# Optimization experiments

Measured on AMD Instinct MI355X. Metric: run time of the kernel, lower is better.

## Reference

```python
import jax, jax.numpy as jnp
import numpy as np

B, L, D, H = 2, 2048, 1024, 16
DK = D // H


def setup_inputs() -> dict:
    key = jax.random.key(0)
    ks = jax.random.split(key, 13)
    s = 1.0 / np.sqrt(D)
    return {
        "q": jax.random.normal(ks[0], (B, L, D), jnp.float32),
        "k": jax.random.normal(ks[1], (B, L, D), jnp.float32),
        "v": jax.random.normal(ks[2], (B, L, D), jnp.float32),
        "mask": jax.random.randint(ks[3], (B, L, L), 0, 2, jnp.int32),
        "Wq": jax.random.normal(ks[4], (D, D), jnp.float32) * s,
        "bq": jnp.zeros((D,), jnp.float32),
        "Wk": jax.random.normal(ks[5], (D, D), jnp.float32) * s,
        "bk": jnp.zeros((D,), jnp.float32),
        "Wv": jax.random.normal(ks[6], (D, D), jnp.float32) * s,
        "bv": jnp.zeros((D,), jnp.float32),
        "Wo": jax.random.normal(ks[7], (D, D), jnp.float32) * s,
        "bo": jnp.zeros((D,), jnp.float32),
    }


def reference(q, k, v, mask, Wq, bq, Wk, bk, Wv, bv, Wo, bo):
    # projections: [B, L, D] -> [B, L, H, DK]
    qh = (q @ Wq + bq).reshape(B, L, H, DK)
    kh = (k @ Wk + bk).reshape(B, L, H, DK)
    vh = (v @ Wv + bv).reshape(B, L, H, DK)
    # scores scaled by d_model (module passes model_dim=d_model, not sqrt(d_k))
    attn = jnp.einsum("bqhd,bkhd->bhqk", qh, kh) / D
    attn = jnp.where(mask[:, None, :, :] == 0, jnp.float32(-1e9), attn)
    attn = jax.nn.softmax(attn, axis=-1)  # [B, H, Lq, Lk]
    ctx = jnp.einsum("bhqk,bkhd->bqhd", attn, vh)  # [B, Lq, H, DK]
    out = ctx.reshape(B, L, D) @ Wo + bo
    # original returns attn flattened head-major: [H*B, Lq, Lk]
    attn_out = attn.transpose(1, 0, 2, 3).reshape(H * B, L, L)
    return out, attn_out
```

## Files before the change

kernel.cpp:

```cpp
#include <hip/hip_runtime.h>
#include <cstdint>

typedef unsigned short u16;
typedef unsigned long long u64;
typedef __attribute__((ext_vector_type(8))) short short8;
typedef __attribute__((ext_vector_type(4))) float floatx4;

#define DEV __device__ __forceinline__

#define GLD16(gp, lp)                                                          \
  __builtin_amdgcn_global_load_lds(                                            \
      (const __attribute__((address_space(1))) void*)(gp),                     \
      (__attribute__((address_space(3))) void*)(lp), 16, 0, 0)

DEV u16 f2bf(float f) {
  union { float f; uint32_t u; } x; x.f = f;
  uint32_t r = x.u + 0x7fffu + ((x.u >> 16) & 1u);
  return (u16)(r >> 16);
}


__global__ __launch_bounds__(256) void pack_mask(
    const int* __restrict__ mask, u64* __restrict__ mw) {
  const int lane = threadIdx.x & 63;
  int gw = (blockIdx.x * 256 + threadIdx.x) >> 6;
  const int nwaves = (gridDim.x * 256) >> 6;
  const int total = (2 * 2048 * 2048) / 64;
  for (int c = gw; c < total; c += nwaves) {
    int v = mask[(size_t)c * 64 + lane];
    u64 b = __ballot(v != 0);
    if (lane == 0) mw[c] = b;
  }
}

__global__ __launch_bounds__(256) void transpose_w(
    const float* __restrict__ s0, const float* __restrict__ s1,
    const float* __restrict__ s2, const float* __restrict__ s3,
    u16* __restrict__ d0, u16* __restrict__ d1,
    u16* __restrict__ d2, u16* __restrict__ d3) {
  const float* S; u16* D;
  switch (blockIdx.z) {
    case 0: S = s0; D = d0; break;
    case 1: S = s1; D = d1; break;
    case 2: S = s2; D = d2; break;
    default: S = s3; D = d3; break;
  }
  __shared__ u16 t[64][68];
  const int tid = threadIdx.x;
  const int r0 = blockIdx.y * 64, c0 = blockIdx.x * 64;
#pragma unroll
  for (int i = 0; i < 4; ++i) {
    int idx = i * 256 + tid;
    int r = idx >> 4, c = (idx & 15) * 4;
    float4 v = *(const float4*)(S + (size_t)(r0 + r) * 1024 + c0 + c);
    t[r][c] = f2bf(v.x); t[r][c + 1] = f2bf(v.y);
    t[r][c + 2] = f2bf(v.z); t[r][c + 3] = f2bf(v.w);
  }
  __syncthreads();
#pragma unroll
  for (int i = 0; i < 4; ++i) {
    int idx = i * 256 + tid;
    int r = idx >> 4, c = (idx & 15) * 4;
    ushort4 v;
    v.x = t[c][r]; v.y = t[c + 1][r]; v.z = t[c + 2][r]; v.w = t[c + 3][r];
    *(ushort4*)(D + (size_t)(c0 + r) * 1024 + r0 + c) = v;
  }
}

__global__ __launch_bounds__(256) void cvt3(
    const float* __restrict__ q, const float* __restrict__ k,
    const float* __restrict__ v, u16* __restrict__ dst) {
  const float* S = (blockIdx.z == 0) ? q : (blockIdx.z == 1) ? k : v;
  u16* D = dst + (size_t)blockIdx.z * (4u << 20);
  int i = (blockIdx.x * 256 + threadIdx.x) * 4;
  float4 val = *(const float4*)(S + i);
  ushort4 o;
  o.x = f2bf(val.x); o.y = f2bf(val.y); o.z = f2bf(val.z); o.w = f2bf(val.w);
  *(ushort4*)(D + i) = o;
}

__global__ __launch_bounds__(256, 3) void gemm_k(
    const u16* xb3, const u16* wts,
    const float* __restrict__ bq, const float* __restrict__ bk,
    const float* __restrict__ bv, const float* __restrict__ bo,
    u16* __restrict__ qh, u16* __restrict__ kh, u16* __restrict__ vt,
    const u16* ctx, float* __restrict__ out, int phase) {
  __shared__ __align__(16) u16 As[128 * 64];
  __shared__ __align__(16) u16 Bs[128 * 64];
  const int tid = threadIdx.x;
  const int wave = tid >> 6, lane = tid & 63;
  const int quad = lane >> 4, l16 = lane & 15;
  const int wm = (wave >> 1) * 64, wn = (wave & 1) * 64;

  int m0, n0, mode;
  const u16 *X, *Wt; const float* bias;
  u16* outb; float* outf;
  if (phase == 0) {
    int flat = blockIdx.x + 32 * (blockIdx.y + 8 * blockIdx.z);
    int xcd = flat & 7, idx = flat >> 3;
    int g = xcd * 3 + (idx >> 5);
    int z = g >> 3;
    m0 = (idx & 31) * 128; n0 = (g & 7) * 128;
    X = xb3 + (size_t)z * (4u << 20);
    Wt = wts + (size_t)z * (1u << 20);
    bias = (z == 0) ? bq : (z == 1) ? bk : bv;
    outb = (z == 0) ? qh : (z == 1) ? kh : vt;
    outf = nullptr;
    mode = (z == 2) ? 1 : 0;
  } else {
    int flat = blockIdx.x + 32 * blockIdx.y;
    int xcd = flat & 7, idx = flat >> 3;
    m0 = (xcd * 4 + (idx >> 3)) * 128; n0 = (idx & 7) * 128;
    X = ctx; Wt = wts + 3 * (size_t)(1u << 20);
    bias = bo; outb = nullptr; outf = out; mode = 2;
  }

  floatx4 acc[4][4];
#pragma unroll
  for (int i = 0; i < 4; ++i)
#pragma unroll
    for (int j = 0; j < 4; ++j) acc[i][j] = (floatx4){0.f, 0.f, 0.f, 0.f};

  for (int k0 = 0; k0 < 1024; k0 += 64) {
#pragma unroll
    for (int r = 0; r < 4; ++r) {
      int c = r * 256 + tid;
      int row = c >> 3, off = (c & 7) * 8;
      GLD16(X + (size_t)(m0 + row) * 1024 + k0 + off, As + c * 8);
      GLD16(Wt + (size_t)(n0 + row) * 1024 + k0 + off, Bs + c * 8);
    }
    __syncthreads();
#pragma unroll
    for (int kk = 0; kk < 64; kk += 32) {
      short8 a[4], b[4];
#pragma unroll
      for (int i = 0; i < 4; ++i)
        a[i] = *(const short8*)(As + (wm + i * 16 + l16) * 64 + kk + quad * 8);
#pragma unroll
      for (int i = 0; i < 4; ++i)
        b[i] = *(const short8*)(Bs + (wn + i * 16 + l16) * 64 + kk + quad * 8);
#pragma unroll
      for (int mi = 0; mi < 4; ++mi)
#pragma unroll
        for (int ni = 0; ni < 4; ++ni)
          acc[mi][ni] = __builtin_amdgcn_mfma_f32_16x16x32_bf16(
              a[mi], b[ni], acc[mi][ni], 0, 0, 0);
    }
    __syncthreads();
  }

#pragma unroll
  for (int mi = 0; mi < 4; ++mi) {
#pragma unroll
    for (int ni = 0; ni < 4; ++ni) {
      const int gn = n0 + wn + ni * 16 + l16;
      const float bv_ = bias[gn];
#pragma unroll
      for (int reg = 0; reg < 4; ++reg) {
        const int gm = m0 + wm + mi * 16 + quad * 4 + reg;
        const float v = acc[mi][ni][reg] + bv_;
        if (mode == 2) {
          __builtin_nontemporal_store(v, outf + (size_t)gm * 1024 + gn);
        } else {
          int bb = gm >> 11, l = gm & 2047, hh = gn >> 6, dk = gn & 63;
          size_t addr = (mode == 0)
              ? (((size_t)(bb * 16 + hh) * 2048 + l) * 64 + dk)
              : (((size_t)(bb * 16 + hh) * 64 + dk) * 2048 + l);
          outb[addr] = f2bf(v);
        }
      }
    }
  }
}

__global__ __launch_bounds__(256, 2) void attn_fused(
    const u16* __restrict__ qh, const u16* __restrict__ kh,
    const u16* __restrict__ vt, const u64* __restrict__ mw,
    float* __restrict__ attn_out, u16* __restrict__ ctx) {
  const int tid = threadIdx.x;
  const int wave = tid >> 6, lane = tid & 63;
  const int quad = lane >> 4, l16 = lane & 15;

  const int flat = blockIdx.x + 32 * (blockIdx.y + 16 * blockIdx.z);
  const int xcd = flat & 7, idx = flat >> 3;
  const int hb = xcd * 4 + (idx >> 5);
  const int q0 = (idx & 31) * 64;
  const int h = hb & 15, b = hb >> 4;
  const int bh = b * 16 + h;

  __shared__ __align__(16) u16 Qs[64 * 72];
  __shared__ __align__(16) u16 Ks[128 * 72];
  __shared__ __align__(16) u16 Vs[64 * 136];
  __shared__ __align__(16) u16 Ps[64 * 136];
  __shared__ float red[4][64];
  __shared__ float rinvs[64];

  const u16* qbase = qh + ((size_t)bh * 2048 + q0) * 64;
  const u16* kbase = kh + (size_t)bh * 2048 * 64;
  const u16* vbase = vt + (size_t)bh * 64 * 2048;
  const u64* mwrow = mw + ((size_t)b * 2048 + q0) * 32;
  float* abase = attn_out + ((size_t)(h * 2 + b) * 2048 + q0) * 2048;

#pragma unroll
  for (int r = 0; r < 2; ++r) {
    int c = r * 256 + tid;
    int row = c >> 3, off = (c & 7) * 8;
    uint4 vv = *(const uint4*)(qbase + (size_t)c * 8);
    *(uint4*)(Qs + row * 72 + off) = vv;
  }

  float rs[4] = {0.f, 0.f, 0.f, 0.f};

  for (int kt = 0; kt < 16; ++kt) {
#pragma unroll
    for (int r = 0; r < 4; ++r) {
      int c = r * 256 + tid;
      int row = c >> 3, off = (c & 7) * 8;
      uint4 vv = *(const uint4*)(kbase + (size_t)kt * 8192 + c * 8);
      *(uint4*)(Ks + row * 72 + off) = vv;
    }
    __syncthreads();

    floatx4 st[2][4];
#pragma unroll
    for (int i = 0; i < 2; ++i)
#pragma unroll
      for (int j = 0; j < 4; ++j) st[i][j] = (floatx4){0.f, 0.f, 0.f, 0.f};
#pragma unroll
    for (int kk = 0; kk < 64; kk += 32) {
      short8 a[2], bqf[4];
#pragma unroll
      for (int ki = 0; ki < 2; ++ki)
        a[ki] = *(const short8*)(Ks + (wave * 32 + ki * 16 + l16) * 72 + kk + quad * 8);
#pragma unroll
      for (int qi = 0; qi < 4; ++qi)
        bqf[qi] = *(const short8*)(Qs + (qi * 16 + l16) * 72 + kk + quad * 8);
#pragma unroll
      for (int ki = 0; ki < 2; ++ki)
#pragma unroll
        for (int qi = 0; qi < 4; ++qi)
          st[ki][qi] = __builtin_amdgcn_mfma_f32_16x16x32_bf16(
              a[ki], bqf[qi], st[ki][qi], 0, 0, 0);
    }

#pragma unroll
    for (int qi = 0; qi < 4; ++qi) {
      u64 w = mwrow[(size_t)(qi * 16 + l16) * 32 + kt * 2 + (wave >> 1)];
#pragma unroll
      for (int ki = 0; ki < 2; ++ki) {
        int bb0 = (wave & 1) * 32 + ki * 16 + quad * 4;
#pragma unroll
        for (int reg = 0; reg < 4; ++reg) {
          float sv = st[ki][qi][reg] * (1.0f / 1024.0f);
          rs[qi] += ((w >> (bb0 + reg)) & 1) ? __expf(sv) : 0.f;
        }
      }
    }
    __syncthreads();
  }

#pragma unroll
  for (int qi = 0; qi < 4; ++qi) {
    float vsum = rs[qi];
    vsum += __shfl_xor(vsum, 16, 64);
    vsum += __shfl_xor(vsum, 32, 64);
    rs[qi] = vsum;
  }
  if (quad == 0) {
#pragma unroll
    for (int qi = 0; qi < 4; ++qi) red[wave][qi * 16 + l16] = rs[qi];
  }
  __syncthreads();
  if (tid < 64) {
    float s = red[0][tid] + red[1][tid] + red[2][tid] + red[3][tid];
    rinvs[tid] = (s > 0.f) ? (1.0f / s) : -1.0f;
  }
  __syncthreads();

  float inv[4];
#pragma unroll
  for (int qi = 0; qi < 4; ++qi) inv[qi] = rinvs[qi * 16 + l16];

  floatx4 cacc[4];
#pragma unroll
  for (int i = 0; i < 4; ++i) cacc[i] = (floatx4){0.f, 0.f, 0.f, 0.f};

  for (int kt = 0; kt < 16; ++kt) {
#pragma unroll
    for (int r = 0; r < 4; ++r) {
      int c = r * 256 + tid;
      int row = c >> 3, off = (c & 7) * 8;
      uint4 vv = *(const uint4*)(kbase + (size_t)kt * 8192 + c * 8);
      *(uint4*)(Ks + row * 72 + off) = vv;
      int dk = c >> 4, ko = (c & 15) * 8;
      uint4 wv = *(const uint4*)(vbase + (size_t)dk * 2048 + kt * 128 + ko);
      *(uint4*)(Vs + dk * 136 + ko) = wv;
    }
    __syncthreads();

    floatx4 st[2][4];
#pragma unroll
    for (int i = 0; i < 2; ++i)
#pragma unroll
      for (int j = 0; j < 4; ++j) st[i][j] = (floatx4){0.f, 0.f, 0.f, 0.f};
#pragma unroll
    for (int kk = 0; kk < 64; kk += 32) {
      short8 a[2], bqf[4];
#pragma unroll
      for (int ki = 0; ki < 2; ++ki)
        a[ki] = *(const short8*)(Ks + (wave * 32 + ki * 16 + l16) * 72 + kk + quad * 8);
#pragma unroll
      for (int qi = 0; qi < 4; ++qi)
        bqf[qi] = *(const short8*)(Qs + (qi * 16 + l16) * 72 + kk + quad * 8);
#pragma unroll
      for (int ki = 0; ki < 2; ++ki)
#pragma unroll
        for (int qi = 0; qi < 4; ++qi)
          st[ki][qi] = __builtin_amdgcn_mfma_f32_16x16x32_bf16(
              a[ki], bqf[qi], st[ki][qi], 0, 0, 0);
    }

#pragma unroll
    for (int qi = 0; qi < 4; ++qi) {
      int row = qi * 16 + l16;
      u64 w = mwrow[(size_t)row * 32 + kt * 2 + (wave >> 1)];
      float iv = inv[qi];
#pragma unroll
      for (int ki = 0; ki < 2; ++ki) {
        int bb0 = (wave & 1) * 32 + ki * 16 + quad * 4;
        int keyl = wave * 32 + ki * 16 + quad * 4;
        floatx4 pv; ushort4 pb;
#pragma unroll
        for (int reg = 0; reg < 4; ++reg) {
          float sv = st[ki][qi][reg] * (1.0f / 1024.0f);
          float p = (iv < 0.f) ? (1.0f / 2048.0f)
                               : (((w >> (bb0 + reg)) & 1) ? __expf(sv) * iv : 0.f);
          pv[reg] = p;
          ((u16*)&pb)[reg] = f2bf(p);
        }
        __builtin_nontemporal_store(
            pv, (floatx4*)(abase + (size_t)row * 2048 + kt * 128 + keyl));
        *(ushort4*)(Ps + row * 136 + keyl) = pb;
      }
    }
    __syncthreads();

#pragma unroll
    for (int ks = 0; ks < 4; ++ks) {
      short8 a[4];
#pragma unroll
      for (int mi = 0; mi < 4; ++mi)
        a[mi] = *(const short8*)(Ps + (mi * 16 + l16) * 136 + ks * 32 + quad * 8);
      short8 bb = *(const short8*)(Vs + (wave * 16 + l16) * 136 + ks * 32 + quad * 8);
#pragma unroll
      for (int mi = 0; mi < 4; ++mi)
        cacc[mi] = __builtin_amdgcn_mfma_f32_16x16x32_bf16(a[mi], bb, cacc[mi], 0, 0, 0);
    }
    __syncthreads();
  }

#pragma unroll
  for (int mi = 0; mi < 4; ++mi)
#pragma unroll
    for (int reg = 0; reg < 4; ++reg) {
      int row = q0 + mi * 16 + quad * 4 + reg;
      int col = h * 64 + wave * 16 + l16;
      ctx[(size_t)(b * 2048 + row) * 1024 + col] = f2bf(cacc[mi][reg]);
    }
}

extern "C" void kernel_launch(void* const* d_in, const int* in_sizes, int n_in,
                              void* d_out, int out_size, void* d_ws, size_t ws_size,
                              hipStream_t stream) {
  const float* q    = (const float*)d_in[0];
  const float* k    = (const float*)d_in[1];
  const float* v    = (const float*)d_in[2];
  const int*   mask = (const int*)d_in[3];
  const float* Wq   = (const float*)d_in[4];
  const float* bq   = (const float*)d_in[5];
  const float* Wk   = (const float*)d_in[6];
  const float* bk   = (const float*)d_in[7];
  const float* Wv   = (const float*)d_in[8];
  const float* bv   = (const float*)d_in[9];
  const float* Wo   = (const float*)d_in[10];
  const float* bo   = (const float*)d_in[11];

  float* out  = (float*)d_out;
  float* attn = out + (size_t)4096 * 1024;

  const size_t M = 1u << 20;
  u16* wtq = (u16*)d_ws;
  u16* wtk = wtq + M;
  u16* wtv = wtk + M;
  u16* wto = wtv + M;
  u16* xb3 = wto + M;
  u16* qh  = xb3 + 12 * M;
  u16* kh  = qh + 4 * M;
  u16* vt  = kh + 4 * M;
  u64* mw  = (u64*)(vt + 4 * M);
  u16* ctx = xb3;

  pack_mask<<<dim3(512), 256, 0, stream>>>(mask, mw);
  transpose_w<<<dim3(16, 16, 4), 256, 0, stream>>>(Wq, Wk, Wv, Wo, wtq, wtk, wtv, wto);
  cvt3<<<dim3(4096, 1, 3), 256, 0, stream>>>(q, k, v, xb3);

  gemm_k<<<dim3(32, 8, 3), 256, 0, stream>>>(xb3, wtq, bq, bk, bv, bo,
                                             qh, kh, vt, ctx, out, 0);
  attn_fused<<<dim3(32, 16, 2), 256, 0, stream>>>(qh, kh, vt, mw, attn, ctx);
  gemm_k<<<dim3(32, 8, 1), 256, 0, stream>>>(xb3, wtq, bq, bk, bv, bo,
                                             qh, kh, vt, ctx, out, 1);
}
```

Before: 844.7 us.

## Register-prefetch K/V/mask tiles in attention and split output GEMM into smaller tiles

The attention kernel now prefetches the next K and V tiles and mask words into registers while the current tile is computed. It replaces the double __syncthreads with custom barriers plus an explicit lgkmcnt wait, and raises wave priority around the MFMA sections. The output projection becomes its own kernel with 64x128 tiles and 512 blocks, to give better occupancy and CU coverage than 256 blocks of 128x128. The cost is higher register pressure from the prefetch buffers, and the hand-written barriers carry a correctness risk if a wait is missed.

```diff
diff --git a/kernel.cpp b/kernel.cpp
--- a/kernel.cpp
+++ b/kernel.cpp
@@ -12,6 +12,20 @@
   __builtin_amdgcn_global_load_lds(                                            \
       (const __attribute__((address_space(1))) void*)(gp),                     \
       (__attribute__((address_space(3))) void*)(lp), 16, 0, 0)
+
+#define BAR()                                                                  \
+  do {                                                                         \
+    asm volatile("" ::: "memory");                                             \
+    __builtin_amdgcn_s_barrier();                                              \
+    asm volatile("" ::: "memory");                                             \
+  } while (0)
+#define LGKM0_BAR()                                                            \
+  do {                                                                         \
+    asm volatile("s_waitcnt lgkmcnt(0)" ::: "memory");                         \
+    __builtin_amdgcn_s_barrier();                                              \
+    asm volatile("" ::: "memory");                                             \
+    __builtin_amdgcn_sched_barrier(0);                                         \
+  } while (0)
 
 DEV u16 f2bf(float f) {
   union { float f; uint32_t u; } x; x.f = f;
@@ -79,12 +93,11 @@
   *(ushort4*)(D + i) = o;
 }
 
-__global__ __launch_bounds__(256, 3) void gemm_k(
+__global__ __launch_bounds__(256, 3) void gemm_qkv(
     const u16* xb3, const u16* wts,
     const float* __restrict__ bq, const float* __restrict__ bk,
-    const float* __restrict__ bv, const float* __restrict__ bo,
-    u16* __restrict__ qh, u16* __restrict__ kh, u16* __restrict__ vt,
-    const u16* ctx, float* __restrict__ out, int phase) {
+    const float* __restrict__ bv,
+    u16* __restrict__ qh, u16* __restrict__ kh, u16* __restrict__ vt) {
   __shared__ __align__(16) u16 As[128 * 64];
   __shared__ __align__(16) u16 Bs[128 * 64];
   const int tid = threadIdx.x;
@@ -92,28 +105,16 @@
   const int quad = lane >> 4, l16 = lane & 15;
   const int wm = (wave >> 1) * 64, wn = (wave & 1) * 64;
 
-  int m0, n0, mode;
-  const u16 *X, *Wt; const float* bias;
-  u16* outb; float* outf;
-  if (phase == 0) {
-    int flat = blockIdx.x + 32 * (blockIdx.y + 8 * blockIdx.z);
-    int xcd = flat & 7, idx = flat >> 3;
-    int g = xcd * 3 + (idx >> 5);
-    int z = g >> 3;
-    m0 = (idx & 31) * 128; n0 = (g & 7) * 128;
-    X = xb3 + (size_t)z * (4u << 20);
-    Wt = wts + (size_t)z * (1u << 20);
-    bias = (z == 0) ? bq : (z == 1) ? bk : bv;
-    outb = (z == 0) ? qh : (z == 1) ? kh : vt;
-    outf = nullptr;
-    mode = (z == 2) ? 1 : 0;
-  } else {
-    int flat = blockIdx.x + 32 * blockIdx.y;
-    int xcd = flat & 7, idx = flat >> 3;
-    m0 = (xcd * 4 + (idx >> 3)) * 128; n0 = (idx & 7) * 128;
-    X = ctx; Wt = wts + 3 * (size_t)(1u << 20);
-    bias = bo; outb = nullptr; outf = out; mode = 2;
-  }
+  int flat = blockIdx.x + 32 * (blockIdx.y + 8 * blockIdx.z);
+  int xcd = flat & 7, idx = flat >> 3;
+  int g = xcd * 3 + (idx >> 5);
+  int z = g >> 3;
+  int m0 = (idx & 31) * 128, n0 = (g & 7) * 128;
+  const u16* X = xb3 + (size_t)z * (4u << 20);
+  const u16* Wt = wts + (size_t)z * (1u << 20);
+  const float* bias = (z == 0) ? bq : (z == 1) ? bk : bv;
+  u16* outb = (z == 0) ? qh : (z == 1) ? kh : vt;
+  int mode = (z == 2) ? 1 : 0;
 
   floatx4 acc[4][4];
 #pragma unroll
@@ -159,15 +160,81 @@
       for (int reg = 0; reg < 4; ++reg) {
         const int gm = m0 + wm + mi * 16 + quad * 4 + reg;
         const float v = acc[mi][ni][reg] + bv_;
-        if (mode == 2) {
-          __builtin_nontemporal_store(v, outf + (size_t)gm * 1024 + gn);
-        } else {
-          int bb = gm >> 11, l = gm & 2047, hh = gn >> 6, dk = gn & 63;
-          size_t addr = (mode == 0)
-              ? (((size_t)(bb * 16 + hh) * 2048 + l) * 64 + dk)
-              : (((size_t)(bb * 16 + hh) * 64 + dk) * 2048 + l);
-          outb[addr] = f2bf(v);
-        }
+        int bb = gm >> 11, l = gm & 2047, hh = gn >> 6, dk = gn & 63;
+        size_t addr = (mode == 0)
+            ? (((size_t)(bb * 16 + hh) * 2048 + l) * 64 + dk)
+            : (((size_t)(bb * 16 + hh) * 64 + dk) * 2048 + l);
+        outb[addr] = f2bf(v);
+      }
+    }
+  }
+}
+
+__global__ __launch_bounds__(256, 2) void gemm_out(
+    const u16* __restrict__ X, const u16* __restrict__ Wt,
+    const float* __restrict__ bias, float* __restrict__ out) {
+  __shared__ __align__(16) u16 As[64 * 64];
+  __shared__ __align__(16) u16 Bs[128 * 64];
+  const int tid = threadIdx.x;
+  const int wave = tid >> 6, lane = tid & 63;
+  const int quad = lane >> 4, l16 = lane & 15;
+  const int wm = (wave >> 1) * 32, wn = (wave & 1) * 64;
+
+  int flat = blockIdx.x;
+  int xcd = flat & 7, idx = flat >> 3;
+  int m0 = (xcd * 8 + (idx >> 3)) * 64;
+  int n0 = (idx & 7) * 128;
+
+  floatx4 acc[2][4];
+#pragma unroll
+  for (int i = 0; i < 2; ++i)
+#pragma unroll
+    for (int j = 0; j < 4; ++j) acc[i][j] = (floatx4){0.f, 0.f, 0.f, 0.f};
+
+  for (int k0 = 0; k0 < 1024; k0 += 64) {
+#pragma unroll
+    for (int r = 0; r < 2; ++r) {
+      int c = r * 256 + tid;
+      int row = c >> 3, off = (c & 7) * 8;
+      GLD16(X + (size_t)(m0 + row) * 1024 + k0 + off, As + c * 8);
+    }
+#pragma unroll
+    for (int r = 0; r < 4; ++r) {
+      int c = r * 256 + tid;
+      int row = c >> 3, off = (c & 7) * 8;
+      GLD16(Wt + (size_t)(n0 + row) * 1024 + k0 + off, Bs + c * 8);
+    }
+    __syncthreads();
+#pragma unroll
+    for (int kk = 0; kk < 64; kk += 32) {
+      short8 a[2], b[4];
+#pragma unroll
+      for (int i = 0; i < 2; ++i)
+        a[i] = *(const short8*)(As + (wm + i * 16 + l16) * 64 + kk + quad * 8);
+#pragma unroll
+      for (int i = 0; i < 4; ++i)
+        b[i] = *(const short8*)(Bs + (wn + i * 16 + l16) * 64 + kk + quad * 8);
+#pragma unroll
+      for (int mi = 0; mi < 2; ++mi)
+#pragma unroll
+        for (int ni = 0; ni < 4; ++ni)
+          acc[mi][ni] = __builtin_amdgcn_mfma_f32_16x16x32_bf16(
+              a[mi], b[ni], acc[mi][ni], 0, 0, 0);
+    }
+    __syncthreads();
+  }
+
+#pragma unroll
+  for (int mi = 0; mi < 2; ++mi) {
+#pragma unroll
+    for (int ni = 0; ni < 4; ++ni) {
+      const int gn = n0 + wn + ni * 16 + l16;
+      const float bv_ = bias[gn];
+#pragma unroll
+      for (int reg = 0; reg < 4; ++reg) {
+        const int gm = m0 + wm + mi * 16 + quad * 4 + reg;
+        __builtin_nontemporal_store(acc[mi][ni][reg] + bv_,
+                                    out + (size_t)gm * 1024 + gn);
       }
     }
   }
@@ -209,23 +276,44 @@
     *(uint4*)(Qs + row * 72 + off) = vv;
   }
 
+  uint4 kreg[4];
+#pragma unroll
+  for (int r = 0; r < 4; ++r)
+    kreg[r] = *(const uint4*)(kbase + (size_t)(r * 256 + tid) * 8);
+  u64 wreg[4];
+#pragma unroll
+  for (int qi = 0; qi < 4; ++qi)
+    wreg[qi] = mwrow[(size_t)(qi * 16 + l16) * 32 + (wave >> 1)];
+
   float rs[4] = {0.f, 0.f, 0.f, 0.f};
 
   for (int kt = 0; kt < 16; ++kt) {
+    BAR();
 #pragma unroll
     for (int r = 0; r < 4; ++r) {
       int c = r * 256 + tid;
-      int row = c >> 3, off = (c & 7) * 8;
-      uint4 vv = *(const uint4*)(kbase + (size_t)kt * 8192 + c * 8);
-      *(uint4*)(Ks + row * 72 + off) = vv;
-    }
-    __syncthreads();
+      *(uint4*)(Ks + (c >> 3) * 72 + (c & 7) * 8) = kreg[r];
+    }
+    u64 wcur[4];
+#pragma unroll
+    for (int qi = 0; qi < 4; ++qi) wcur[qi] = wreg[qi];
+    if (kt < 15) {
+#pragma unroll
+      for (int r = 0; r < 4; ++r)
+        kreg[r] = *(const uint4*)(kbase + (size_t)(kt + 1) * 8192 +
+                                  (size_t)(r * 256 + tid) * 8);
+#pragma unroll
+      for (int qi = 0; qi < 4; ++qi)
+        wreg[qi] = mwrow[(size_t)(qi * 16 + l16) * 32 + (kt + 1) * 2 + (wave >> 1)];
+    }
+    LGKM0_BAR();
 
     floatx4 st[2][4];
 #pragma unroll
     for (int i = 0; i < 2; ++i)
 #pragma unroll
       for (int j = 0; j < 4; ++j) st[i][j] = (floatx4){0.f, 0.f, 0.f, 0.f};
+    __builtin_amdgcn_s_setprio(1);
 #pragma unroll
     for (int kk = 0; kk < 64; kk += 32) {
       short8 a[2], bqf[4];
@@ -242,10 +330,11 @@
           st[ki][qi] = __builtin_amdgcn_mfma_f32_16x16x32_bf16(
               a[ki], bqf[qi], st[ki][qi], 0, 0, 0);
     }
+    __builtin_amdgcn_s_setprio(0);
 
 #pragma unroll
     for (int qi = 0; qi < 4; ++qi) {
-      u64 w = mwrow[(size_t)(qi * 16 + l16) * 32 + kt * 2 + (wave >> 1)];
+      u64 w = wcur[qi];
 #pragma unroll
       for (int ki = 0; ki < 2; ++ki) {
         int bb0 = (wave & 1) * 32 + ki * 16 + quad * 4;
@@ -256,8 +345,19 @@
         }
       }
     }
-    __syncthreads();
-  }
+  }
+
+  uint4 vreg[4];
+#pragma unroll
+  for (int r = 0; r < 4; ++r) {
+    int c = r * 256 + tid;
+    kreg[r] = *(const uint4*)(kbase + (size_t)c * 8);
+    int dk = c >> 4, ko = (c & 15) * 8;
+    vreg[r] = *(const uint4*)(vbase + (size_t)dk * 2048 + ko);
+  }
+#pragma unroll
+  for (int qi = 0; qi < 4; ++qi)
+    wreg[qi] = mwrow[(size_t)(qi * 16 + l16) * 32 + (wave >> 1)];
 
 #pragma unroll
   for (int qi = 0; qi < 4; ++qi) {
@@ -270,12 +370,12 @@
 #pragma unroll
     for (int qi = 0; qi < 4; ++qi) red[wave][qi * 16 + l16] = rs[qi];
   }
-  __syncthreads();
+  LGKM0_BAR();
   if (tid < 64) {
     float s = red[0][tid] + red[1][tid] + red[2][tid] + red[3][tid];
     rinvs[tid] = (s > 0.f) ? (1.0f / s) : -1.0f;
   }
-  __syncthreads();
+  LGKM0_BAR();
 
   float inv[4];
 #pragma unroll
@@ -286,23 +386,37 @@
   for (int i = 0; i < 4; ++i) cacc[i] = (floatx4){0.f, 0.f, 0.f, 0.f};
 
   for (int kt = 0; kt < 16; ++kt) {
+    BAR();
 #pragma unroll
     for (int r = 0; r < 4; ++r) {
       int c = r * 256 + tid;
-      int row = c >> 3, off = (c & 7) * 8;
-      uint4 vv = *(const uint4*)(kbase + (size_t)kt * 8192 + c * 8);
-      *(uint4*)(Ks + row * 72 + off) = vv;
+      *(uint4*)(Ks + (c >> 3) * 72 + (c & 7) * 8) = kreg[r];
       int dk = c >> 4, ko = (c & 15) * 8;
-      uint4 wv = *(const uint4*)(vbase + (size_t)dk * 2048 + kt * 128 + ko);
-      *(uint4*)(Vs + dk * 136 + ko) = wv;
-    }
-    __syncthreads();
+      *(uint4*)(Vs + dk * 136 + ko) = vreg[r];
+    }
+    u64 wcur[4];
+#pragma unroll
+    for (int qi = 0; qi < 4; ++qi) wcur[qi] = wreg[qi];
+    if (kt < 15) {
+#pragma unroll
+      for (int r = 0; r < 4; ++r) {
+        int c = r * 256 + tid;
+        kreg[r] = *(const uint4*)(kbase + (size_t)(kt + 1) * 8192 + (size_t)c * 8);
+        int dk = c >> 4, ko = (c & 15) * 8;
+        vreg[r] = *(const uint4*)(vbase + (size_t)dk * 2048 + (kt + 1) * 128 + ko);
+      }
+#pragma unroll
+      for (int qi = 0; qi < 4; ++qi)
+        wreg[qi] = mwrow[(size_t)(qi * 16 + l16) * 32 + (kt + 1) * 2 + (wave >> 1)];
+    }
+    LGKM0_BAR();
 
     floatx4 st[2][4];
 #pragma unroll
     for (int i = 0; i < 2; ++i)
 #pragma unroll
       for (int j = 0; j < 4; ++j) st[i][j] = (floatx4){0.f, 0.f, 0.f, 0.f};
+    __builtin_amdgcn_s_setprio(1);
 #pragma unroll
     for (int kk = 0; kk < 64; kk += 32) {
       short8 a[2], bqf[4];
@@ -319,11 +433,12 @@
           st[ki][qi] = __builtin_amdgcn_mfma_f32_16x16x32_bf16(
               a[ki], bqf[qi], st[ki][qi], 0, 0, 0);
     }
+    __builtin_amdgcn_s_setprio(0);
 
 #pragma unroll
     for (int qi = 0; qi < 4; ++qi) {
       int row = qi * 16 + l16;
-      u64 w = mwrow[(size_t)row * 32 + kt * 2 + (wave >> 1)];
+      u64 w = wcur[qi];
       float iv = inv[qi];
 #pragma unroll
       for (int ki = 0; ki < 2; ++ki) {
@@ -343,8 +458,9 @@
         *(ushort4*)(Ps + row * 136 + keyl) = pb;
       }
     }
-    __syncthreads();
-
+    LGKM0_BAR();
+
+    __builtin_amdgcn_s_setprio(1);
 #pragma unroll
     for (int ks = 0; ks < 4; ++ks) {
       short8 a[4];
@@ -356,7 +472,7 @@
       for (int mi = 0; mi < 4; ++mi)
         cacc[mi] = __builtin_amdgcn_mfma_f32_16x16x32_bf16(a[mi], bb, cacc[mi], 0, 0, 0);
     }
-    __syncthreads();
+    __builtin_amdgcn_s_setprio(0);
   }
 
 #pragma unroll
@@ -404,9 +520,7 @@
   transpose_w<<<dim3(16, 16, 4), 256, 0, stream>>>(Wq, Wk, Wv, Wo, wtq, wtk, wtv, wto);
   cvt3<<<dim3(4096, 1, 3), 256, 0, stream>>>(q, k, v, xb3);
 
-  gemm_k<<<dim3(32, 8, 3), 256, 0, stream>>>(xb3, wtq, bq, bk, bv, bo,
-                                             qh, kh, vt, ctx, out, 0);
+  gemm_qkv<<<dim3(32, 8, 3), 256, 0, stream>>>(xb3, wtq, bq, bk, bv, qh, kh, vt);
   attn_fused<<<dim3(32, 16, 2), 256, 0, stream>>>(qh, kh, vt, mw, attn, ctx);
-  gemm_k<<<dim3(32, 8, 1), 256, 0, stream>>>(xb3, wtq, bq, bk, bv, bo,
-                                             qh, kh, vt, ctx, out, 1);
-}
+  gemm_out<<<dim3(512), 256, 0, stream>>>(ctx, wto, bo, out);
+}
```

After: 858.8 us. About the same (+1.7%).
